# Performance work log

Hardware: AMD Instinct MI355X
Metric: run time of the kernel (lower is better)

Reference implementation:

```python
import jax, jax.numpy as jnp
import numpy as np

OUT_F, IN_F, RANK = 4096, 4096, 32
N_TOK = 8192  # batch 4 * seq 2048, flattened


def setup_inputs() -> dict:
    key = jax.random.key(0)
    k_x, k_w, k_s, k_a, k_b, k_bias = jax.random.split(key, 6)
    x = jax.random.normal(k_x, (N_TOK, IN_F), dtype=jnp.float32)
    # ternary weights in {-1, 0, +1}, stored as int8 buffer
    weight_q = (jax.random.randint(k_w, (OUT_F, IN_F), 0, 3) - 1).astype(jnp.int8)
    # per-output-channel absmean scale, shape [out, 1], positive
    scale = 0.02 + 0.05 * jax.random.uniform(k_s, (OUT_F, 1), dtype=jnp.float32)
    lora_A = 0.01 * jax.random.normal(k_a, (OUT_F, RANK), dtype=jnp.float32)
    lora_B = 0.01 * jax.random.normal(k_b, (RANK, IN_F), dtype=jnp.float32)
    bias = 0.01 * jax.random.normal(k_bias, (OUT_F,), dtype=jnp.float32)
    return {"x": x, "weight_q": weight_q, "scale": scale,
            "lora_A": lora_A, "lora_B": lora_B, "bias": bias}


def reference(x, weight_q, scale, lora_A, lora_B, bias):
    # out = (x @ W_q^T) * scale_per_out_channel + x @ B^T @ A^T + bias
    Wq = weight_q.astype(x.dtype)                       # dequantize {-1,0,1}
    out = jnp.einsum('ti,oi->to', x, Wq) * scale.reshape(1, -1)
    # low-rank LoRA residual: (x @ B^T) @ A^T, rank-RANK bottleneck
    out = out + (x @ lora_B.T) @ lora_A.T
    out = out + bias
    return out
```

## Files before the change

### kernel.cpp

```cpp
#include <hip/hip_runtime.h>
#include <stdint.h>

typedef unsigned short u16;
typedef __attribute__((ext_vector_type(8))) __bf16 bf16x8;
typedef __attribute__((ext_vector_type(4))) float f32x4;

__device__ __forceinline__ u16 f2bf(float f) {
  unsigned int u = __builtin_bit_cast(unsigned int, f);
  u = (u + 0x7FFFu + ((u >> 16) & 1u)) >> 16;
  return (u16)u;
}
__device__ __forceinline__ u16 tern2bf(int s) {
  return s == 0 ? (u16)0 : (s > 0 ? (u16)0x3F80 : (u16)0xBF80);
}

#define GLOAD_LDS16(g, l)                                                          \
  __builtin_amdgcn_global_load_lds((__attribute__((address_space(1))) void*)(g),   \
                                   (__attribute__((address_space(3))) void*)(l),   \
                                   16, 0, 0)

#define M_TOK 8192
#define N_OUT 4096
#define K_IN  4096
#define RANK  32

#define WS_XB    0ull
#define WS_WB    67108864ull
#define WS_BB    100663296ull
#define WS_A32   100925440ull
#define WS_T32   101187584ull
#define WS_TPART 101711872ull
#define WS_FLAG  110100480ull

__global__ void k_convert_x(const float4* __restrict__ x, ushort4* __restrict__ xb, int n4) {
  int stride = gridDim.x * blockDim.x;
  for (int i = blockIdx.x * blockDim.x + threadIdx.x; i < n4; i += stride) {
    float4 v = x[i];
    ushort4 o;
    o.x = f2bf(v.x); o.y = f2bf(v.y); o.z = f2bf(v.z); o.w = f2bf(v.w);
    xb[i] = o;
  }
}

__global__ void k_detect_wtype(const int* __restrict__ w, int* __restrict__ flag) {
  int v = w[threadIdx.x];
  bool ok = (v >= -1 && v <= 1);
  unsigned long long m = __ballot(ok);
  if (threadIdx.x == 0) *flag = (m == ~0ull) ? 1 : 0;
}

__global__ void k_convert_w(const void* __restrict__ wq, const int* __restrict__ flag,
                            ushort4* __restrict__ wb, int n4) {
  int is32 = *flag;
  int stride = gridDim.x * blockDim.x;
  for (int i = blockIdx.x * blockDim.x + threadIdx.x; i < n4; i += stride) {
    int s0, s1, s2, s3;
    if (is32) {
      int4 c = ((const int4*)wq)[i];
      s0 = c.x; s1 = c.y; s2 = c.z; s3 = c.w;
    } else {
      char4 c = ((const char4*)wq)[i];
      s0 = c.x; s1 = c.y; s2 = c.z; s3 = c.w;
    }
    ushort4 o;
    o.x = tern2bf(s0); o.y = tern2bf(s1); o.z = tern2bf(s2); o.w = tern2bf(s3);
    wb[i] = o;
  }
}

__global__ void k_prep_B(const float* __restrict__ loraB, u16* __restrict__ bb) {
  int idx = blockIdx.x * blockDim.x + threadIdx.x;
  if (idx < RANK * K_IN) bb[idx] = f2bf(loraB[idx]);
}

__global__ void k_prep_A(const float* __restrict__ loraA, const float* __restrict__ scale,
                         u16* __restrict__ a32) {
  int idx = blockIdx.x * blockDim.x + threadIdx.x;
  if (idx >= N_OUT * RANK) return;
  int o = idx >> 5;
  a32[idx] = f2bf(loraA[idx] / scale[o]);
}

__global__ __launch_bounds__(256) void k_lora_T(const u16* __restrict__ xb,
                                                const u16* __restrict__ bb,
                                                float* __restrict__ tpart) {
  __shared__ u16 As[256 * 32];
  __shared__ u16 Bs[32 * 32];
  int mt = blockIdx.x >> 3;
  int ks = blockIdx.x & 7;
  int tid = threadIdx.x, lane = tid & 63, wave = tid >> 6;
  int m0 = mt * 256;
  int kbase0 = ks * 512;
  f32x4 acc[4][2] = {};
  for (int step = 0; step < 16; ++step) {
    int kb = kbase0 + step * 32;
    __syncthreads();
#pragma unroll
    for (int i = 0; i < 4; ++i) {
      const u16* src = xb + (size_t)(m0 + i * 64 + (tid >> 2)) * K_IN + kb + (tid & 3) * 8;
      GLOAD_LDS16(src, &As[i * 2048 + tid * 8]);
    }
    if (tid < 128) {
      const u16* src = bb + (size_t)(tid >> 2) * K_IN + kb + (tid & 3) * 8;
      GLOAD_LDS16(src, &Bs[tid * 8]);
    }
    __syncthreads();
    bf16x8 b[2];
#pragma unroll
    for (int ni = 0; ni < 2; ++ni)
      b[ni] = *(const bf16x8*)&Bs[(ni * 16 + (lane & 15)) * 32 + (lane >> 4) * 8];
#pragma unroll
    for (int mi = 0; mi < 4; ++mi) {
      bf16x8 a = *(const bf16x8*)&As[(wave * 64 + mi * 16 + (lane & 15)) * 32 + (lane >> 4) * 8];
      acc[mi][0] = __builtin_amdgcn_mfma_f32_16x16x32_bf16(a, b[0], acc[mi][0], 0, 0, 0);
      acc[mi][1] = __builtin_amdgcn_mfma_f32_16x16x32_bf16(a, b[1], acc[mi][1], 0, 0, 0);
    }
  }
#pragma unroll
  for (int mi = 0; mi < 4; ++mi)
#pragma unroll
    for (int ni = 0; ni < 2; ++ni)
#pragma unroll
      for (int r = 0; r < 4; ++r) {
        int row = m0 + wave * 64 + mi * 16 + (lane >> 4) * 4 + r;
        int col = ni * 16 + (lane & 15);
        tpart[((size_t)ks * M_TOK + row) * RANK + col] = acc[mi][ni][r];
      }
}

__global__ void k_reduce_T(const float* __restrict__ tpart, u16* __restrict__ t32) {
  int idx = blockIdx.x * blockDim.x + threadIdx.x;
  if (idx >= M_TOK * RANK) return;
  int t = idx >> 5, r = idx & 31;
  float v = 0.f;
#pragma unroll
  for (int s = 0; s < 8; ++s) v += tpart[((size_t)s * M_TOK + t) * RANK + r];
  t32[idx] = f2bf(v);
}

__global__ __launch_bounds__(512, 2) void k_gemm8(const u16* __restrict__ xb,
                                                  const u16* __restrict__ wb,
                                                  const u16* __restrict__ t32,
                                                  const u16* __restrict__ a32,
                                                  const float* __restrict__ scale,
                                                  const float* __restrict__ bias,
                                                  float* __restrict__ out) {
  __shared__ u16 As[4][8192];
  __shared__ u16 Bs[4][8192];
  const int tid = threadIdx.x;
  const int l = tid & 63, w = tid >> 6;
  const int wm = w >> 2, wn = w & 3;
  const int bid = blockIdx.x;
  const int swz = (bid & 7) * 64 + (bid >> 3);
  const int m0 = (swz >> 4) * 256, n0 = (swz & 15) * 256;

  const int srow0 = (w * 2 + 0) * 16 + (l >> 2);
  const int srow1 = (w * 2 + 1) * 16 + (l >> 2);
  const int scx = ((l & 3) ^ ((l >> 3) & 3)) * 8;
  const int ldst0 = (w * 2 + 0) * 512 + l * 8;
  const int ldst1 = (w * 2 + 1) * 512 + l * 8;
  const int r15 = l & 15;
  const int cxr = (((l >> 4) ^ ((r15 >> 1) & 3)) * 8);

  f32x4 acc[8][4] = {};

  auto stageA = [&](int ts) {
    int tc = ts < 128 ? ts : 128;
    const u16 *s0, *s1;
    if (tc < 128) {
      s0 = xb + (size_t)(m0 + srow0) * K_IN + tc * 32 + scx;
      s1 = xb + (size_t)(m0 + srow1) * K_IN + tc * 32 + scx;
    } else {
      s0 = t32 + (size_t)(m0 + srow0) * RANK + scx;
      s1 = t32 + (size_t)(m0 + srow1) * RANK + scx;
    }
    u16* d = &As[ts & 3][0];
    GLOAD_LDS16(s0, d + ldst0);
    GLOAD_LDS16(s1, d + ldst1);
  };
  auto stageB = [&](int ts) {
    int tc = ts < 128 ? ts : 128;
    const u16 *s0, *s1;
    if (tc < 128) {
      s0 = wb + (size_t)(n0 + srow0) * K_IN + tc * 32 + scx;
      s1 = wb + (size_t)(n0 + srow1) * K_IN + tc * 32 + scx;
    } else {
      s0 = a32 + (size_t)(n0 + srow0) * RANK + scx;
      s1 = a32 + (size_t)(n0 + srow1) * RANK + scx;
    }
    u16* d = &Bs[ts & 3][0];
    GLOAD_LDS16(s0, d + ldst0);
    GLOAD_LDS16(s1, d + ldst1);
  };

  stageA(0); stageB(0);
  stageA(1); stageB(1);
  stageA(2); stageB(2);
  asm volatile("s_waitcnt vmcnt(8)" ::: "memory");
  __builtin_amdgcn_s_barrier();

#pragma unroll 1
  for (int t = 0; t < 129; ++t) {
    const u16* Asl = &As[t & 3][0];
    const u16* Bsl = &Bs[t & 3][0];
    bf16x8 af0[4], bfr[4];
    {
      const int ab = (wm * 128 + r15) * 32 + cxr;
#pragma unroll
      for (int mi = 0; mi < 4; ++mi) af0[mi] = *(const bf16x8*)&Asl[ab + mi * 512];
      const int bb2 = (wn * 64 + r15) * 32 + cxr;
#pragma unroll
      for (int nj = 0; nj < 4; ++nj) bfr[nj] = *(const bf16x8*)&Bsl[bb2 + nj * 512];
    }
    stageA(t + 3);
    __builtin_amdgcn_s_barrier();
    asm volatile("s_waitcnt lgkmcnt(0)" ::: "memory");
    __builtin_amdgcn_s_setprio(1);
#pragma unroll
    for (int mi = 0; mi < 4; ++mi)
#pragma unroll
      for (int nj = 0; nj < 4; ++nj)
        acc[mi][nj] = __builtin_amdgcn_mfma_f32_16x16x32_bf16(af0[mi], bfr[nj], acc[mi][nj], 0, 0, 0);
    __builtin_amdgcn_s_setprio(0);
    __builtin_amdgcn_s_barrier();
    bf16x8 af1[4];
    {
      const int ab = (wm * 128 + 64 + r15) * 32 + cxr;
#pragma unroll
      for (int mi = 0; mi < 4; ++mi) af1[mi] = *(const bf16x8*)&Asl[ab + mi * 512];
    }
    stageB(t + 3);
    asm volatile("s_waitcnt vmcnt(8)" ::: "memory");
    __builtin_amdgcn_s_barrier();
    asm volatile("s_waitcnt lgkmcnt(0)" ::: "memory");
    __builtin_amdgcn_s_setprio(1);
#pragma unroll
    for (int mi = 0; mi < 4; ++mi)
#pragma unroll
      for (int nj = 0; nj < 4; ++nj)
        acc[4 + mi][nj] = __builtin_amdgcn_mfma_f32_16x16x32_bf16(af1[mi], bfr[nj], acc[4 + mi][nj], 0, 0, 0);
    __builtin_amdgcn_s_setprio(0);
    __builtin_amdgcn_s_barrier();
  }

#pragma unroll
  for (int nj = 0; nj < 4; ++nj) {
    int col = n0 + wn * 64 + nj * 16 + r15;
    float s = scale[col], bv = bias[col];
#pragma unroll
    for (int fi = 0; fi < 8; ++fi) {
      int row = m0 + wm * 128 + (fi >> 2) * 64 + (fi & 3) * 16 + (l >> 4) * 4;
#pragma unroll
      for (int r = 0; r < 4; ++r)
        out[(size_t)(row + r) * N_OUT + col] = acc[fi][nj][r] * s + bv;
    }
  }
}

extern "C" void kernel_launch(void* const* d_in, const int* in_sizes, int n_in,
                              void* d_out, int out_size, void* d_ws, size_t ws_size,
                              hipStream_t stream) {
  const float* x     = (const float*)d_in[0];
  const void*  wq    = d_in[1];
  const float* scale = (const float*)d_in[2];
  const float* loraA = (const float*)d_in[3];
  const float* loraB = (const float*)d_in[4];
  const float* bias  = (const float*)d_in[5];
  float* out = (float*)d_out;

  char* ws = (char*)d_ws;
  u16*   xb    = (u16*)(ws + WS_XB);
  u16*   wbuf  = (u16*)(ws + WS_WB);
  u16*   bb    = (u16*)(ws + WS_BB);
  u16*   a32   = (u16*)(ws + WS_A32);
  u16*   t32   = (u16*)(ws + WS_T32);
  float* tpart = (float*)(ws + WS_TPART);
  int*   flag  = (int*)(ws + WS_FLAG);

  k_convert_x<<<2048, 256, 0, stream>>>((const float4*)x, (ushort4*)xb, M_TOK * K_IN / 4);
  k_detect_wtype<<<1, 64, 0, stream>>>((const int*)wq, flag);
  k_convert_w<<<2048, 256, 0, stream>>>(wq, flag, (ushort4*)wbuf, N_OUT * K_IN / 4);
  k_prep_B<<<512, 256, 0, stream>>>(loraB, bb);
  k_prep_A<<<512, 256, 0, stream>>>(loraA, scale, a32);
  k_lora_T<<<256, 256, 0, stream>>>(xb, bb, tpart);
  k_reduce_T<<<1024, 256, 0, stream>>>(tpart, t32);
  k_gemm8<<<512, 512, 0, stream>>>(xb, wbuf, t32, a32, scale, bias, out);

  (void)in_sizes; (void)n_in; (void)out_size; (void)ws_size;
}
```

Baseline: 340.3 us.

## Unroll K-loop by four with fixed LDS slots and one barrier per tile

The main K loop is unrolled four times so each iteration uses compile-time LDS slot offsets, and global source pointers are advanced incrementally instead of recomputing addresses each tile. The four barriers and explicit lgkmcnt waits per tile are cut to a single barrier at the end of each tile. The LoRA rank tile and the drain tiles are peeled into an epilogue, with vmcnt waits that taper off. The aim is less synchronisation stall and less address arithmetic in the hot loop. The trade-off is larger code size, and ordering between LDS reads and refills now depends on the single barrier.

```diff
diff --git a/kernel.cpp b/kernel.cpp
--- a/kernel.cpp
+++ b/kernel.cpp
@@ -164,84 +164,93 @@
 
   f32x4 acc[8][4] = {};
 
-  auto stageA = [&](int ts) {
-    int tc = ts < 128 ? ts : 128;
-    const u16 *s0, *s1;
-    if (tc < 128) {
-      s0 = xb + (size_t)(m0 + srow0) * K_IN + tc * 32 + scx;
-      s1 = xb + (size_t)(m0 + srow1) * K_IN + tc * 32 + scx;
-    } else {
-      s0 = t32 + (size_t)(m0 + srow0) * RANK + scx;
-      s1 = t32 + (size_t)(m0 + srow1) * RANK + scx;
-    }
-    u16* d = &As[ts & 3][0];
-    GLOAD_LDS16(s0, d + ldst0);
-    GLOAD_LDS16(s1, d + ldst1);
-  };
-  auto stageB = [&](int ts) {
-    int tc = ts < 128 ? ts : 128;
-    const u16 *s0, *s1;
-    if (tc < 128) {
-      s0 = wb + (size_t)(n0 + srow0) * K_IN + tc * 32 + scx;
-      s1 = wb + (size_t)(n0 + srow1) * K_IN + tc * 32 + scx;
-    } else {
-      s0 = a32 + (size_t)(n0 + srow0) * RANK + scx;
-      s1 = a32 + (size_t)(n0 + srow1) * RANK + scx;
-    }
-    u16* d = &Bs[ts & 3][0];
-    GLOAD_LDS16(s0, d + ldst0);
-    GLOAD_LDS16(s1, d + ldst1);
-  };
-
-  stageA(0); stageB(0);
-  stageA(1); stageB(1);
-  stageA(2); stageB(2);
+  u16* AsF = &As[0][0];
+  u16* BsF = &Bs[0][0];
+  const u16* axs0 = xb + (size_t)(m0 + srow0) * K_IN + scx;
+  const u16* axs1 = xb + (size_t)(m0 + srow1) * K_IN + scx;
+  const u16* bxs0 = wb + (size_t)(n0 + srow0) * K_IN + scx;
+  const u16* bxs1 = wb + (size_t)(n0 + srow1) * K_IN + scx;
+
+#pragma unroll
+  for (int ts = 0; ts < 3; ++ts) {
+    GLOAD_LDS16(axs0 + ts * 32, AsF + ts * 8192 + ldst0);
+    GLOAD_LDS16(axs1 + ts * 32, AsF + ts * 8192 + ldst1);
+    GLOAD_LDS16(bxs0 + ts * 32, BsF + ts * 8192 + ldst0);
+    GLOAD_LDS16(bxs1 + ts * 32, BsF + ts * 8192 + ldst1);
+  }
   asm volatile("s_waitcnt vmcnt(8)" ::: "memory");
-  __builtin_amdgcn_s_barrier();
+  asm volatile("s_barrier" ::: "memory");
+
+  const int abase = (wm * 128 + r15) * 32 + cxr;
+  const int bbase = (wn * 64 + r15) * 32 + cxr;
+
+  const u16* ap0 = axs0 + 96;
+  const u16* ap1 = axs1 + 96;
+  const u16* bp0 = bxs0 + 96;
+  const u16* bp1 = bxs1 + 96;
+
+#define TILE(SLOT, STAGE_A, STAGE_B, WAIT, BAR)                                     \
+  {                                                                                 \
+    const u16* Asl = AsF + (SLOT) * 8192;                                           \
+    const u16* Bsl = BsF + (SLOT) * 8192;                                           \
+    bf16x8 a0[4], bfr[4], a1[4];                                                    \
+    _Pragma("unroll") for (int mi = 0; mi < 4; ++mi)                                \
+        a0[mi] = *(const bf16x8*)&Asl[abase + mi * 512];                            \
+    _Pragma("unroll") for (int nj = 0; nj < 4; ++nj)                                \
+        bfr[nj] = *(const bf16x8*)&Bsl[bbase + nj * 512];                           \
+    STAGE_A                                                                         \
+    __builtin_amdgcn_s_setprio(1);                                                  \
+    _Pragma("unroll") for (int mi = 0; mi < 4; ++mi)                                \
+    _Pragma("unroll") for (int nj = 0; nj < 4; ++nj)                                \
+        acc[mi][nj] =                                                               \
+            __builtin_amdgcn_mfma_f32_16x16x32_bf16(a0[mi], bfr[nj], acc[mi][nj], 0, 0, 0); \
+    __builtin_amdgcn_s_setprio(0);                                                  \
+    _Pragma("unroll") for (int mi = 0; mi < 4; ++mi)                                \
+        a1[mi] = *(const bf16x8*)&Asl[abase + 2048 + mi * 512];                     \
+    STAGE_B                                                                         \
+    WAIT                                                                            \
+    __builtin_amdgcn_s_setprio(1);                                                  \
+    _Pragma("unroll") for (int mi = 0; mi < 4; ++mi)                                \
+    _Pragma("unroll") for (int nj = 0; nj < 4; ++nj)                                \
+        acc[4 + mi][nj] =                                                           \
+            __builtin_amdgcn_mfma_f32_16x16x32_bf16(a1[mi], bfr[nj], acc[4 + mi][nj], 0, 0, 0); \
+    __builtin_amdgcn_s_setprio(0);                                                  \
+    BAR                                                                             \
+  }
+
+#define SA(DST)                                                                     \
+  { GLOAD_LDS16(ap0, AsF + (DST) * 8192 + ldst0);                                   \
+    GLOAD_LDS16(ap1, AsF + (DST) * 8192 + ldst1); }
+#define SB(DST)                                                                     \
+  { GLOAD_LDS16(bp0, BsF + (DST) * 8192 + ldst0);                                   \
+    GLOAD_LDS16(bp1, BsF + (DST) * 8192 + ldst1);                                   \
+    ap0 += 32; ap1 += 32; bp0 += 32; bp1 += 32; }
+#define W8  asm volatile("s_waitcnt vmcnt(8)" ::: "memory");
+#define W4  asm volatile("s_waitcnt vmcnt(4)" ::: "memory");
+#define W0  asm volatile("s_waitcnt vmcnt(0)" ::: "memory");
+#define BARR asm volatile("s_barrier" ::: "memory");
 
 #pragma unroll 1
-  for (int t = 0; t < 129; ++t) {
-    const u16* Asl = &As[t & 3][0];
-    const u16* Bsl = &Bs[t & 3][0];
-    bf16x8 af0[4], bfr[4];
-    {
-      const int ab = (wm * 128 + r15) * 32 + cxr;
-#pragma unroll
-      for (int mi = 0; mi < 4; ++mi) af0[mi] = *(const bf16x8*)&Asl[ab + mi * 512];
-      const int bb2 = (wn * 64 + r15) * 32 + cxr;
-#pragma unroll
-      for (int nj = 0; nj < 4; ++nj) bfr[nj] = *(const bf16x8*)&Bsl[bb2 + nj * 512];
-    }
-    stageA(t + 3);
-    __builtin_amdgcn_s_barrier();
-    asm volatile("s_waitcnt lgkmcnt(0)" ::: "memory");
-    __builtin_amdgcn_s_setprio(1);
-#pragma unroll
-    for (int mi = 0; mi < 4; ++mi)
-#pragma unroll
-      for (int nj = 0; nj < 4; ++nj)
-        acc[mi][nj] = __builtin_amdgcn_mfma_f32_16x16x32_bf16(af0[mi], bfr[nj], acc[mi][nj], 0, 0, 0);
-    __builtin_amdgcn_s_setprio(0);
-    __builtin_amdgcn_s_barrier();
-    bf16x8 af1[4];
-    {
-      const int ab = (wm * 128 + 64 + r15) * 32 + cxr;
-#pragma unroll
-      for (int mi = 0; mi < 4; ++mi) af1[mi] = *(const bf16x8*)&Asl[ab + mi * 512];
-    }
-    stageB(t + 3);
-    asm volatile("s_waitcnt vmcnt(8)" ::: "memory");
-    __builtin_amdgcn_s_barrier();
-    asm volatile("s_waitcnt lgkmcnt(0)" ::: "memory");
-    __builtin_amdgcn_s_setprio(1);
-#pragma unroll
-    for (int mi = 0; mi < 4; ++mi)
-#pragma unroll
-      for (int nj = 0; nj < 4; ++nj)
-        acc[4 + mi][nj] = __builtin_amdgcn_mfma_f32_16x16x32_bf16(af1[mi], bfr[nj], acc[4 + mi][nj], 0, 0, 0);
-    __builtin_amdgcn_s_setprio(0);
-    __builtin_amdgcn_s_barrier();
-  }
+  for (int t = 0; t < 124; t += 4) {
+    TILE(0, SA(3), SB(3), W8, BARR)
+    TILE(1, SA(0), SB(0), W8, BARR)
+    TILE(2, SA(1), SB(1), W8, BARR)
+    TILE(3, SA(2), SB(2), W8, BARR)
+  }
+  TILE(0, SA(3), SB(3), W8, BARR)
+  {
+    const u16* la0 = t32 + (size_t)(m0 + srow0) * RANK + scx;
+    const u16* la1 = t32 + (size_t)(m0 + srow1) * RANK + scx;
+    const u16* lb0 = a32 + (size_t)(n0 + srow0) * RANK + scx;
+    const u16* lb1 = a32 + (size_t)(n0 + srow1) * RANK + scx;
+    TILE(1,
+         { GLOAD_LDS16(la0, AsF + 0 * 8192 + ldst0); GLOAD_LDS16(la1, AsF + 0 * 8192 + ldst1); },
+         { GLOAD_LDS16(lb0, BsF + 0 * 8192 + ldst0); GLOAD_LDS16(lb1, BsF + 0 * 8192 + ldst1); },
+         W8, BARR)
+  }
+  TILE(2, , , W4, BARR)
+  TILE(3, , , W0, BARR)
+  TILE(0, , , , )
 
 #pragma unroll
   for (int nj = 0; nj < 4; ++nj) {
```

Result: faster. 325.8 us (-4.3%).
